# Kernel optimization log

Hardware: AMD Instinct MI355X
Metric: run time of the kernel (lower is better)

Reference implementation:

```python
import jax, jax.numpy as jnp
import numpy as np

HIDDEN = 1024
HEADS = 16
HEAD_SIZE = HIDDEN // HEADS


def setup_inputs() -> dict:
    key = jax.random.key(0)
    k0, k1, k2, k3 = jax.random.split(key, 4)
    scale = 1.0 / np.sqrt(HIDDEN)
    return {
        "input_data": jax.random.normal(k0, (4, 4096, HIDDEN), dtype=jnp.float32),
        "W0": jax.random.normal(k1, (HIDDEN, HIDDEN), dtype=jnp.float32) * scale,
        "W1": jax.random.normal(k2, (HIDDEN, HIDDEN), dtype=jnp.float32) * scale,
        "W2": jax.random.normal(k3, (HIDDEN, HIDDEN), dtype=jnp.float32) * scale,
    }


def reference(input_data, W0, W1, W2):
    b, s, _ = input_data.shape
    k, h = HEADS, HEAD_SIZE
    # torch.nn.Linear(bias=False): y = x @ W.T
    out = input_data @ W0.T          # [b, s, hidden]
    out1 = input_data @ W1.T
    out2 = input_data @ W2.T
    # reshape to heads; cummax over the sequence axis (axis=1 here, which
    # matches cummax(dim=2) on the permuted (b,k,s,h) layout in torch)
    out_h = out.reshape(b, s, k, h)
    out1_h = out1.reshape(b, s, k, h)
    cm = jax.lax.associative_scan(jnp.maximum, (out_h + out1_h) / jnp.sqrt(jnp.float32(h)), axis=1)
    cm = cm.reshape(b, s, k * h)
    out = (cm + out2) * cm + out1
    return out
```

## Files before the change

kernel.cpp:

```cpp
#include <hip/hip_runtime.h>
#include <cstdint>
#include <cstddef>

#define HIDDEN 1024
#define BATCH 4
#define SEQ 4096
#define M_ROWS (BATCH * SEQ)
#define K_DIM 1024
#define SUBCHUNK 32
#define NSUB (SEQ / SUBCHUNK)

typedef __bf16 bf16_t;
typedef __bf16 v8bf __attribute__((ext_vector_type(8)));
typedef float v4f __attribute__((ext_vector_type(4)));

__device__ __forceinline__ unsigned short f32_to_bf16(float f) {
  unsigned int u = __float_as_uint(f);
  u += 0x7fffu + ((u >> 16) & 1u);
  return (unsigned short)(u >> 16);
}
__device__ __forceinline__ float bf16_to_f32(unsigned short u) {
  return __uint_as_float((unsigned int)u << 16);
}

__global__ void convert_kernel(const float* __restrict__ X,
                               const float* __restrict__ W0,
                               const float* __restrict__ W1,
                               const float* __restrict__ W2,
                               unsigned short* __restrict__ Xb,
                               unsigned short* __restrict__ Wb) {
  int bx = blockIdx.x;
  if (bx < 16384) {
    int i = bx * 256 + threadIdx.x;
    float4 f = ((const float4*)X)[i];
    ushort4 u;
    u.x = f32_to_bf16(f.x); u.y = f32_to_bf16(f.y);
    u.z = f32_to_bf16(f.z); u.w = f32_to_bf16(f.w);
    ((ushort4*)Xb)[i] = u;
  } else {
    int i = (bx - 16384) * 256 + threadIdx.x;
    int mat = i >> 18;
    int off = i & 0x3FFFF;
    float4 f;
    if (mat == 0) {
      float4 a = ((const float4*)W0)[off];
      float4 b = ((const float4*)W1)[off];
      f.x = (a.x + b.x) * 0.125f; f.y = (a.y + b.y) * 0.125f;
      f.z = (a.z + b.z) * 0.125f; f.w = (a.w + b.w) * 0.125f;
    } else {
      const float* src = (mat == 1) ? W1 : W2;
      f = ((const float4*)src)[off];
    }
    ushort4 u;
    u.x = f32_to_bf16(f.x); u.y = f32_to_bf16(f.y);
    u.z = f32_to_bf16(f.z); u.w = f32_to_bf16(f.w);
    ((ushort4*)Wb)[i] = u;
  }
}


__global__ __launch_bounds__(512, 2) void gemm_s_kernel(
    const bf16_t* __restrict__ A, const bf16_t* __restrict__ B,
    unsigned short* __restrict__ Lp, float* __restrict__ cmax) {
  extern __shared__ __align__(16) char smem[];

  const int tid = threadIdx.x;
  const int wave = tid >> 6;
  const int lane = tid & 63;
  const int quad = lane >> 4;
  const int r16 = lane & 15;
  const int wr = wave >> 2;
  const int wc = wave & 3;

  const int orig = (int)blockIdx.x;
  const int swz = (orig & 7) * 32 + (orig >> 3);
  const int bx = swz & 3;
  const int mt = swz >> 2;
  const int mtile0 = mt * 256;
  const int nbase = bx * 256;

  const int l3 = lane >> 3;
  const int lc = lane & 7;
  const size_t laneOff = (size_t)l3 * K_DIM + (size_t)((lc ^ l3) << 3);
  const bf16_t* Ag = A + (size_t)(mtile0 + wave * 8) * K_DIM + laneOff;
  const bf16_t* Bg = B + (size_t)(nbase + wave * 8) * K_DIM + laneOff;

  const int aRow = (wr * 128 + r16) * 128;
  const int bRow = (wc * 64 + r16) * 128;
  const int cxor = (r16 & 7) * 16;
  const int qx = quad * 16;

  v4f acc[8][4];
#pragma unroll
  for (int i = 0; i < 8; ++i)
#pragma unroll
    for (int j = 0; j < 4; ++j) acc[i][j] = (v4f)(0.0f);

  v8bf afr[4];
  v8bf bfr[4][2];

#define STG_A(d, q, kt) __builtin_amdgcn_global_load_lds( \
    (__attribute__((address_space(1))) void*)(Ag + (size_t)(q) * (64 * K_DIM) + (size_t)(kt) * 64), \
    (__attribute__((address_space(3))) void*)(smem + (d) * 32768 + (q) * 8192 + wave * 1024), 16, 0, 0)
#define STG_B(d, q, kt) __builtin_amdgcn_global_load_lds( \
    (__attribute__((address_space(1))) void*)(Bg + (size_t)(q) * (64 * K_DIM) + (size_t)(kt) * 64), \
    (__attribute__((address_space(3))) void*)(smem + 65536 + (d) * 32768 + (q) * 8192 + wave * 1024), 16, 0, 0)
#define LDA(d, i, kk) (*(const v8bf*)(smem + (d) * 32768 + aRow + (i) * 2048 + (((kk) * 64 + qx) ^ cxor)))
#define LDB(d, j, kk) (*(const v8bf*)(smem + 65536 + (d) * 32768 + bRow + (j) * 2048 + (((kk) * 64 + qx) ^ cxor)))
#define RD_A(d, ih, kk) { _Pragma("unroll") for (int ii = 0; ii < 4; ++ii) afr[ii] = LDA(d, (ih) * 4 + ii, kk); }
#define RD_B(d, kk) { _Pragma("unroll") for (int j = 0; j < 4; ++j) bfr[j][kk] = LDB(d, j, kk); }
#define MM(ih, kk) \
  __builtin_amdgcn_s_barrier(); \
  asm volatile("s_waitcnt lgkmcnt(0)" ::: "memory"); \
  __builtin_amdgcn_s_setprio(1); \
  { _Pragma("unroll") for (int ii = 0; ii < 4; ++ii) { _Pragma("unroll") for (int j = 0; j < 4; ++j) \
      acc[(ih) * 4 + ii][j] = __builtin_amdgcn_mfma_f32_16x16x32_bf16(afr[ii], bfr[j][(kk)], acc[(ih) * 4 + ii][j], 0, 0, 0); } } \
  __builtin_amdgcn_s_setprio(0);
#define BAR() __builtin_amdgcn_s_barrier()
#define WAITV(n) asm volatile("s_waitcnt vmcnt(" #n ")" ::: "memory")

  STG_A(0, 0, 0); STG_A(0, 1, 0); STG_A(0, 2, 0); STG_A(0, 3, 0);
  STG_B(0, 0, 0); STG_B(0, 1, 0); STG_B(0, 2, 0); STG_B(0, 3, 0);
  STG_A(1, 0, 1); STG_A(1, 2, 1); STG_B(1, 0, 1); STG_B(1, 1, 1);
  WAITV(4);
  BAR();

  for (int it = 0; it < 7; ++it) {
    const int t1 = 2 * it + 1, t2 = t1 + 1, t3 = t1 + 2;
    RD_A(0, 0, 0); RD_B(0, 0);
    STG_B(1, 2, t1); STG_B(1, 3, t1);
    MM(0, 0); BAR();
    RD_B(0, 1); RD_A(0, 0, 1);
    STG_A(1, 1, t1); STG_A(1, 3, t1);
    MM(0, 1); BAR();
    RD_A(0, 1, 0);
    STG_A(0, 0, t2); STG_A(0, 2, t2);
    MM(1, 0); BAR();
    RD_A(0, 1, 1);
    STG_B(0, 0, t2); STG_B(0, 1, t2);
    MM(1, 1); WAITV(4); BAR();
    RD_A(1, 0, 0); RD_B(1, 0);
    STG_B(0, 2, t2); STG_B(0, 3, t2);
    MM(0, 0); BAR();
    RD_B(1, 1); RD_A(1, 0, 1);
    STG_A(0, 1, t2); STG_A(0, 3, t2);
    MM(0, 1); BAR();
    RD_A(1, 1, 0);
    STG_A(1, 0, t3); STG_A(1, 2, t3);
    MM(1, 0); BAR();
    RD_A(1, 1, 1);
    STG_B(1, 0, t3); STG_B(1, 1, t3);
    MM(1, 1); WAITV(4); BAR();
  }
  RD_A(0, 0, 0); RD_B(0, 0);
  STG_B(1, 2, 15); STG_B(1, 3, 15);
  MM(0, 0); BAR();
  RD_B(0, 1); RD_A(0, 0, 1);
  STG_A(1, 1, 15); STG_A(1, 3, 15);
  MM(0, 1); BAR();
  RD_A(0, 1, 0); MM(1, 0); BAR();
  RD_A(0, 1, 1); MM(1, 1); WAITV(0); BAR();
  RD_A(1, 0, 0); RD_B(1, 0); MM(0, 0); BAR();
  RD_B(1, 1); RD_A(1, 0, 1); MM(0, 1); BAR();
  RD_A(1, 1, 0); MM(1, 0); BAR();
  RD_A(1, 1, 1); MM(1, 1);

#undef STG_A
#undef STG_B
#undef LDA
#undef LDB
#undef RD_A
#undef RD_B
#undef MM
#undef BAR
#undef WAITV

  const int ncol0 = bx * 256;
  const int bidx = mtile0 >> 12;
  const int sub0 = (mtile0 & 4095) >> 5;
  ushort4* Lq4 = (ushort4*)Lp;
#pragma unroll
  for (int s = 0; s < 4; ++s) {
#pragma unroll
    for (int j = 0; j < 4; ++j) {
      float c0[4], c1[4];
      c0[0] = acc[s * 2][j][0];
      c1[0] = acc[s * 2 + 1][j][0];
#pragma unroll
      for (int r = 1; r < 4; ++r) {
        c0[r] = fmaxf(c0[r - 1], acc[s * 2][j][r]);
        c1[r] = fmaxf(c1[r - 1], acc[s * 2 + 1][j][r]);
      }
      float t0 = c0[3], t1 = c1[3], u;
      u = __shfl_up(t0, 16); if (quad >= 1) t0 = fmaxf(t0, u);
      u = __shfl_up(t0, 32); if (quad >= 2) t0 = fmaxf(t0, u);
      u = __shfl_up(t1, 16); if (quad >= 1) t1 = fmaxf(t1, u);
      u = __shfl_up(t1, 32); if (quad >= 2) t1 = fmaxf(t1, u);
      float e0 = __shfl_up(t0, 16); if (quad == 0) e0 = -INFINITY;
      float e1 = __shfl_up(t1, 16); if (quad == 0) e1 = -INFINITY;
      float T0 = __shfl(t0, 48 + r16);
      float T1 = __shfl(t1, 48 + r16);
      const int gfb = mt * 8 + bx * 2 + (wc >> 1);
      const int thrC = (wr * 4 + (wc & 1) * 2 + (j >> 1)) * 64 + lane;
      ushort4 q0, q1;
      q0.x = f32_to_bf16(fmaxf(c0[0], e0));
      q0.y = f32_to_bf16(fmaxf(c0[1], e0));
      q0.z = f32_to_bf16(fmaxf(c0[2], e0));
      q0.w = f32_to_bf16(fmaxf(c0[3], e0));
      float f1 = fmaxf(e1, T0);
      q1.x = f32_to_bf16(fmaxf(c1[0], f1));
      q1.y = f32_to_bf16(fmaxf(c1[1], f1));
      q1.z = f32_to_bf16(fmaxf(c1[2], f1));
      q1.w = f32_to_bf16(fmaxf(c1[3], f1));
      Lq4[((size_t)gfb * 16 + (s * 2 + 0) * 2 + (j & 1)) * 512 + thrC] = q0;
      Lq4[((size_t)gfb * 16 + (s * 2 + 1) * 2 + (j & 1)) * 512 + thrC] = q1;
      if (quad == 0) {
        int sub = sub0 + wr * 4 + s;
        int col = ncol0 + wc * 64 + j * 16 + r16;
        cmax[((size_t)bidx * NSUB + sub) * HIDDEN + col] = fmaxf(T0, T1);
      }
    }
  }
}

__global__ void prefix_kernel(const float* __restrict__ cmax,
                              float* __restrict__ pmax) {
  int col = blockIdx.x * 256 + threadIdx.x;
  int b = blockIdx.y;
  const float* cp = cmax + (size_t)b * NSUB * HIDDEN + col;
  float* pp = pmax + (size_t)b * NSUB * HIDDEN + col;
  float run = -INFINITY;
#pragma unroll 1
  for (int s0 = 0; s0 < NSUB; s0 += 16) {
    float v[16];
#pragma unroll
    for (int i = 0; i < 16; ++i) v[i] = cp[(size_t)(s0 + i) * HIDDEN];
#pragma unroll
    for (int i = 0; i < 16; ++i) {
      pp[(size_t)(s0 + i) * HIDDEN] = run;
      run = fmaxf(run, v[i]);
    }
  }
}

__global__ __launch_bounds__(512, 2) void gemm_f_kernel(
    const bf16_t* __restrict__ A, const bf16_t* __restrict__ B,
    const unsigned short* __restrict__ Lp, const float* __restrict__ pmax,
    float* __restrict__ out) {
  extern __shared__ __align__(16) char smem[];

  const int tid = threadIdx.x;
  const int wave = tid >> 6;
  const int lane = tid & 63;
  const int quad = lane >> 4;
  const int r16 = lane & 15;
  const int wr = wave >> 2;
  const int wc = wave & 3;

  const int orig = (int)blockIdx.x;
  const int swz = (orig & 7) * 64 + (orig >> 3);
  const int mt = swz >> 3;
  const int nt = swz & 7;
  const int mtile0 = mt * 256;
  const int ncol0 = nt * 128;

  const int l3 = lane >> 3;
  const int lc = lane & 7;
  const size_t laneOff = (size_t)l3 * K_DIM + (size_t)((lc ^ l3) << 3);
  const bf16_t* Ag = A + (size_t)(mtile0 + wave * 8) * K_DIM + laneOff;
  const bf16_t* Bg1 = B + (size_t)(1024 + ncol0 + wave * 8) * K_DIM + laneOff;
  const bf16_t* Bg2 = B + (size_t)(2048 + ncol0 + wave * 8) * K_DIM + laneOff;

  const int aRow = (wr * 128 + r16) * 128;
  const int bRow = (wc * 32 + r16) * 128;
  const int cxor = (r16 & 7) * 16;
  const int qx = quad * 16;

  v4f acc1[8][2], acc2[8][2];
#pragma unroll
  for (int i = 0; i < 8; ++i)
#pragma unroll
    for (int j = 0; j < 2; ++j) { acc1[i][j] = (v4f)(0.0f); acc2[i][j] = (v4f)(0.0f); }

  v8bf afr[4];
  v8bf b1fr[2][2], b2fr[2][2];

#define STG2_A(d, q, kt) __builtin_amdgcn_global_load_lds( \
    (__attribute__((address_space(1))) void*)(Ag + (size_t)(q) * (64 * K_DIM) + (size_t)(kt) * 64), \
    (__attribute__((address_space(3))) void*)(smem + (d) * 32768 + (q) * 8192 + wave * 1024), 16, 0, 0)
#define STG2_B1(d, q, kt) __builtin_amdgcn_global_load_lds( \
    (__attribute__((address_space(1))) void*)(Bg1 + (size_t)(q) * (64 * K_DIM) + (size_t)(kt) * 64), \
    (__attribute__((address_space(3))) void*)(smem + 65536 + (d) * 32768 + (q) * 8192 + wave * 1024), 16, 0, 0)
#define STG2_B2(d, q, kt) __builtin_amdgcn_global_load_lds( \
    (__attribute__((address_space(1))) void*)(Bg2 + (size_t)(q) * (64 * K_DIM) + (size_t)(kt) * 64), \
    (__attribute__((address_space(3))) void*)(smem + 65536 + (d) * 32768 + 16384 + (q) * 8192 + wave * 1024), 16, 0, 0)
#define LDA2(d, i, kk) (*(const v8bf*)(smem + (d) * 32768 + aRow + (i) * 2048 + (((kk) * 64 + qx) ^ cxor)))
#define LDB21(d, j, kk) (*(const v8bf*)(smem + 65536 + (d) * 32768 + bRow + (j) * 2048 + (((kk) * 64 + qx) ^ cxor)))
#define LDB22(d, j, kk) (*(const v8bf*)(smem + 65536 + (d) * 32768 + 16384 + bRow + (j) * 2048 + (((kk) * 64 + qx) ^ cxor)))
#define RD2_A(d, ih, kk) { _Pragma("unroll") for (int ii = 0; ii < 4; ++ii) afr[ii] = LDA2(d, (ih) * 4 + ii, kk); }
#define RD2_B(d, kk) { _Pragma("unroll") for (int j = 0; j < 2; ++j) { b1fr[j][kk] = LDB21(d, j, kk); b2fr[j][kk] = LDB22(d, j, kk); } }
#define MM2(ih, kk) \
  __builtin_amdgcn_s_barrier(); \
  asm volatile("s_waitcnt lgkmcnt(0)" ::: "memory"); \
  __builtin_amdgcn_s_setprio(1); \
  { _Pragma("unroll") for (int ii = 0; ii < 4; ++ii) { _Pragma("unroll") for (int j = 0; j < 2; ++j) { \
      acc1[(ih) * 4 + ii][j] = __builtin_amdgcn_mfma_f32_16x16x32_bf16(afr[ii], b1fr[j][(kk)], acc1[(ih) * 4 + ii][j], 0, 0, 0); \
      acc2[(ih) * 4 + ii][j] = __builtin_amdgcn_mfma_f32_16x16x32_bf16(afr[ii], b2fr[j][(kk)], acc2[(ih) * 4 + ii][j], 0, 0, 0); } } } \
  __builtin_amdgcn_s_setprio(0);
#define BAR() __builtin_amdgcn_s_barrier()
#define WAITV(n) asm volatile("s_waitcnt vmcnt(" #n ")" ::: "memory")

  STG2_A(0, 0, 0); STG2_A(0, 1, 0); STG2_A(0, 2, 0); STG2_A(0, 3, 0);
  STG2_B1(0, 0, 0); STG2_B1(0, 1, 0); STG2_B2(0, 0, 0); STG2_B2(0, 1, 0);
  STG2_A(1, 0, 1); STG2_A(1, 2, 1); STG2_B1(1, 0, 1); STG2_B1(1, 1, 1);
  WAITV(4);
  BAR();

  for (int it = 0; it < 7; ++it) {
    const int t1 = 2 * it + 1, t2 = t1 + 1, t3 = t1 + 2;
    RD2_A(0, 0, 0); RD2_B(0, 0);
    STG2_B2(1, 0, t1); STG2_B2(1, 1, t1);
    MM2(0, 0); BAR();
    RD2_B(0, 1); RD2_A(0, 0, 1);
    STG2_A(1, 1, t1); STG2_A(1, 3, t1);
    MM2(0, 1); BAR();
    RD2_A(0, 1, 0);
    STG2_A(0, 0, t2); STG2_A(0, 2, t2);
    MM2(1, 0); BAR();
    RD2_A(0, 1, 1);
    STG2_B1(0, 0, t2); STG2_B1(0, 1, t2);
    MM2(1, 1); WAITV(4); BAR();
    RD2_A(1, 0, 0); RD2_B(1, 0);
    STG2_B2(0, 0, t2); STG2_B2(0, 1, t2);
    MM2(0, 0); BAR();
    RD2_B(1, 1); RD2_A(1, 0, 1);
    STG2_A(0, 1, t2); STG2_A(0, 3, t2);
    MM2(0, 1); BAR();
    RD2_A(1, 1, 0);
    STG2_A(1, 0, t3); STG2_A(1, 2, t3);
    MM2(1, 0); BAR();
    RD2_A(1, 1, 1);
    STG2_B1(1, 0, t3); STG2_B1(1, 1, t3);
    MM2(1, 1); WAITV(4); BAR();
  }
  RD2_A(0, 0, 0); RD2_B(0, 0);
  STG2_B2(1, 0, 15); STG2_B2(1, 1, 15);
  MM2(0, 0); BAR();
  RD2_B(0, 1); RD2_A(0, 0, 1);
  STG2_A(1, 1, 15); STG2_A(1, 3, 15);
  MM2(0, 1); BAR();
  RD2_A(0, 1, 0); MM2(1, 0); BAR();
  RD2_A(0, 1, 1); MM2(1, 1); WAITV(0); BAR();
  RD2_A(1, 0, 0); RD2_B(1, 0); MM2(0, 0); BAR();
  RD2_B(1, 1); RD2_A(1, 0, 1); MM2(0, 1); BAR();
  RD2_A(1, 1, 0); MM2(1, 0); BAR();
  RD2_A(1, 1, 1); MM2(1, 1);

#undef STG2_A
#undef STG2_B1
#undef STG2_B2
#undef LDA2
#undef LDB21
#undef LDB22
#undef RD2_A
#undef RD2_B
#undef MM2
#undef BAR
#undef WAITV

  const int bidx = mtile0 >> 12;
  const int sub0 = (mtile0 & 4095) >> 5;
  const int gfb = mt * 8 + nt;
  const ushort4* Lq4 = (const ushort4*)Lp;
#pragma unroll
  for (int i = 0; i < 8; ++i) {
    const int subr = sub0 + wr * 4 + (i >> 1);
#pragma unroll
    for (int j = 0; j < 2; ++j) {
      const int col = ncol0 + wc * 32 + j * 16 + r16;
      const float pm = pmax[((size_t)bidx * NSUB + subr) * HIDDEN + col];
      const ushort4 q = Lq4[((size_t)gfb * 16 + i * 2 + j) * 512 + tid];
      const int row0 = mtile0 + wr * 128 + i * 16 + quad * 4;
      float m0 = fmaxf(pm, bf16_to_f32(q.x));
      float m1 = fmaxf(pm, bf16_to_f32(q.y));
      float m2 = fmaxf(pm, bf16_to_f32(q.z));
      float m3 = fmaxf(pm, bf16_to_f32(q.w));
      size_t idx = (size_t)row0 * HIDDEN + col;
      out[idx] = (m0 + acc2[i][j][0]) * m0 + acc1[i][j][0];
      out[idx + HIDDEN] = (m1 + acc2[i][j][1]) * m1 + acc1[i][j][1];
      out[idx + 2 * HIDDEN] = (m2 + acc2[i][j][2]) * m2 + acc1[i][j][2];
      out[idx + 3 * HIDDEN] = (m3 + acc2[i][j][3]) * m3 + acc1[i][j][3];
    }
  }
}

extern "C" void kernel_launch(void* const* d_in, const int* in_sizes, int n_in,
                              void* d_out, int out_size, void* d_ws, size_t ws_size,
                              hipStream_t stream) {
  const float* X = (const float*)d_in[0];
  const float* W0 = (const float*)d_in[1];
  const float* W1 = (const float*)d_in[2];
  const float* W2 = (const float*)d_in[3];
  float* out = (float*)d_out;

  char* ws = (char*)d_ws;
  unsigned short* Xb = (unsigned short*)ws;
  unsigned short* Wb = (unsigned short*)(ws + 33554432);
  unsigned short* Lp = (unsigned short*)(ws + 33554432 + 6291456);
  float* cmax = (float*)(ws + 4 * 33554432 + 6291456);
  float* pmax = (float*)(ws + 4 * 33554432 + 6291456 + 2097152);

  convert_kernel<<<19456, 256, 0, stream>>>(X, W0, W1, W2, Xb, Wb);

  gemm_s_kernel<<<256, 512, 131072, stream>>>((const bf16_t*)Xb, (const bf16_t*)Wb,
                                              Lp, cmax);

  dim3 pgrid(4, BATCH);
  prefix_kernel<<<pgrid, 256, 0, stream>>>(cmax, pmax);

  gemm_f_kernel<<<512, 512, 131072, stream>>>((const bf16_t*)Xb, (const bf16_t*)Wb,
                                              Lp, pmax, out);
}
```

Before: 130.6 us.

## Fuse prefix-max scan into final GEMM via atomic tickets and spin-wait

Removes the separate prefix_kernel launch. The first 64 blocks of gemm_f each have wave 0 take a ticket and compute one slice of the per-chunk prefix max, then publish completion through an atomic counter. All blocks spin on that counter before the epilogue, so the scan overlaps the GEMM main loop. The Lp partial-max loads are also issued early into registers, which hides their latency but raises register pressure. The spin-wait depends on the ticketed blocks being resident, and wave 0 of those blocks starts its GEMM work late.

```diff
diff --git a/kernel.cpp b/kernel.cpp
--- a/kernel.cpp
+++ b/kernel.cpp
@@ -28,8 +28,10 @@
                                const float* __restrict__ W1,
                                const float* __restrict__ W2,
                                unsigned short* __restrict__ Xb,
-                               unsigned short* __restrict__ Wb) {
+                               unsigned short* __restrict__ Wb,
+                               int* __restrict__ flags) {
   int bx = blockIdx.x;
+  if (bx == 0 && threadIdx.x == 0) { flags[0] = 0; flags[1] = 0; }
   if (bx < 16384) {
     int i = bx * 256 + threadIdx.x;
     float4 f = ((const float4*)X)[i];
@@ -223,29 +225,10 @@
   }
 }
 
-__global__ void prefix_kernel(const float* __restrict__ cmax,
-                              float* __restrict__ pmax) {
-  int col = blockIdx.x * 256 + threadIdx.x;
-  int b = blockIdx.y;
-  const float* cp = cmax + (size_t)b * NSUB * HIDDEN + col;
-  float* pp = pmax + (size_t)b * NSUB * HIDDEN + col;
-  float run = -INFINITY;
-#pragma unroll 1
-  for (int s0 = 0; s0 < NSUB; s0 += 16) {
-    float v[16];
-#pragma unroll
-    for (int i = 0; i < 16; ++i) v[i] = cp[(size_t)(s0 + i) * HIDDEN];
-#pragma unroll
-    for (int i = 0; i < 16; ++i) {
-      pp[(size_t)(s0 + i) * HIDDEN] = run;
-      run = fmaxf(run, v[i]);
-    }
-  }
-}
-
 __global__ __launch_bounds__(512, 2) void gemm_f_kernel(
     const bf16_t* __restrict__ A, const bf16_t* __restrict__ B,
-    const unsigned short* __restrict__ Lp, const float* __restrict__ pmax,
+    const unsigned short* __restrict__ Lp, const float* __restrict__ cmax,
+    float* __restrict__ pmax, int* __restrict__ flags,
     float* __restrict__ out) {
   extern __shared__ __align__(16) char smem[];
 
@@ -263,6 +246,37 @@
   const int nt = swz & 7;
   const int mtile0 = mt * 256;
   const int ncol0 = nt * 128;
+
+  if (wave == 0) {
+    int ticket = 0;
+    if (lane == 0)
+      ticket = __hip_atomic_fetch_add(&flags[0], 1, __ATOMIC_RELAXED,
+                                      __HIP_MEMORY_SCOPE_AGENT);
+    ticket = __shfl(ticket, 0);
+    if (ticket < 64) {
+      const int pb = ticket >> 4;
+      const int pcol = (ticket & 15) * 64 + lane;
+      const float* cp = cmax + (size_t)pb * NSUB * HIDDEN + pcol;
+      float* pp = pmax + (size_t)pb * NSUB * HIDDEN + pcol;
+      float run = -INFINITY;
+#pragma unroll 1
+      for (int s0 = 0; s0 < NSUB; s0 += 16) {
+        float v[16];
+#pragma unroll
+        for (int i = 0; i < 16; ++i) v[i] = cp[(size_t)(s0 + i) * HIDDEN];
+#pragma unroll
+        for (int i = 0; i < 16; ++i) {
+          pp[(size_t)(s0 + i) * HIDDEN] = run;
+          run = fmaxf(run, v[i]);
+        }
+      }
+      asm volatile("s_waitcnt vmcnt(0)" ::: "memory");
+      __threadfence();
+      if (lane == 0)
+        __hip_atomic_fetch_add(&flags[1], 1, __ATOMIC_RELEASE,
+                               __HIP_MEMORY_SCOPE_AGENT);
+    }
+  }
 
   const int l3 = lane >> 3;
   const int lc = lane & 7;
@@ -351,6 +365,16 @@
   MM2(0, 1); BAR();
   RD2_A(0, 1, 0); MM2(1, 0); BAR();
   RD2_A(0, 1, 1); MM2(1, 1); WAITV(0); BAR();
+
+  const int gfb = mt * 8 + nt;
+  const ushort4* Lq4 = (const ushort4*)Lp;
+  ushort4 lfv[8][2];
+#pragma unroll
+  for (int i = 0; i < 8; ++i)
+#pragma unroll
+    for (int j = 0; j < 2; ++j)
+      lfv[i][j] = Lq4[((size_t)gfb * 16 + i * 2 + j) * 512 + tid];
+
   RD2_A(1, 0, 0); RD2_B(1, 0); MM2(0, 0); BAR();
   RD2_B(1, 1); RD2_A(1, 0, 1); MM2(0, 1); BAR();
   RD2_A(1, 1, 0); MM2(1, 0); BAR();
@@ -368,10 +392,15 @@
 #undef BAR
 #undef WAITV
 
+  if (tid == 0) {
+    while (__hip_atomic_load(&flags[1], __ATOMIC_ACQUIRE,
+                             __HIP_MEMORY_SCOPE_AGENT) < 64)
+      __builtin_amdgcn_s_sleep(2);
+  }
+  __syncthreads();
+
   const int bidx = mtile0 >> 12;
   const int sub0 = (mtile0 & 4095) >> 5;
-  const int gfb = mt * 8 + nt;
-  const ushort4* Lq4 = (const ushort4*)Lp;
 #pragma unroll
   for (int i = 0; i < 8; ++i) {
     const int subr = sub0 + wr * 4 + (i >> 1);
@@ -379,7 +408,7 @@
     for (int j = 0; j < 2; ++j) {
       const int col = ncol0 + wc * 32 + j * 16 + r16;
       const float pm = pmax[((size_t)bidx * NSUB + subr) * HIDDEN + col];
-      const ushort4 q = Lq4[((size_t)gfb * 16 + i * 2 + j) * 512 + tid];
+      const ushort4 q = lfv[i][j];
       const int row0 = mtile0 + wr * 128 + i * 16 + quad * 4;
       float m0 = fmaxf(pm, bf16_to_f32(q.x));
       float m1 = fmaxf(pm, bf16_to_f32(q.y));
@@ -407,17 +436,15 @@
   unsigned short* Xb = (unsigned short*)ws;
   unsigned short* Wb = (unsigned short*)(ws + 33554432);
   unsigned short* Lp = (unsigned short*)(ws + 33554432 + 6291456);
+  int* flags = (int*)(ws + 2 * 33554432 + 6291456);
   float* cmax = (float*)(ws + 4 * 33554432 + 6291456);
   float* pmax = (float*)(ws + 4 * 33554432 + 6291456 + 2097152);
 
-  convert_kernel<<<19456, 256, 0, stream>>>(X, W0, W1, W2, Xb, Wb);
+  convert_kernel<<<19456, 256, 0, stream>>>(X, W0, W1, W2, Xb, Wb, flags);
 
   gemm_s_kernel<<<256, 512, 131072, stream>>>((const bf16_t*)Xb, (const bf16_t*)Wb,
                                               Lp, cmax);
 
-  dim3 pgrid(4, BATCH);
-  prefix_kernel<<<pgrid, 256, 0, stream>>>(cmax, pmax);
-
   gemm_f_kernel<<<512, 512, 131072, stream>>>((const bf16_t*)Xb, (const bf16_t*)Wb,
-                                              Lp, pmax, out);
-}
+                                              Lp, cmax, pmax, flags, out);
+}
```

Result: no change. 132.6 us (+1.5%).
